# Kernel optimization log

Measured on AMD Instinct MI355X. Metric: run time of the kernel, lower is better.

## Reference

```python
import jax, jax.numpy as jnp
import numpy as np

INPUT_SIZE, HIDDEN, OUT = 2, 32, 1

def setup_inputs() -> dict:
    key = jax.random.key(0)
    ks = jax.random.split(key, 8)
    B, T = 2048, 512
    s_ih = 1.0 / np.sqrt(HIDDEN)
    return {
        "x": jax.random.normal(ks[0], (B, T, INPUT_SIZE), dtype=jnp.float32),
        "W_ih": jax.random.uniform(ks[1], (4 * HIDDEN, INPUT_SIZE), minval=-s_ih, maxval=s_ih, dtype=jnp.float32),
        "W_hh": jax.random.uniform(ks[2], (4 * HIDDEN, HIDDEN), minval=-s_ih, maxval=s_ih, dtype=jnp.float32),
        "b_ih": jax.random.uniform(ks[3], (4 * HIDDEN,), minval=-s_ih, maxval=s_ih, dtype=jnp.float32),
        "b_hh": jax.random.uniform(ks[4], (4 * HIDDEN,), minval=-s_ih, maxval=s_ih, dtype=jnp.float32),
        "W_fc": jax.random.uniform(ks[5], (OUT, HIDDEN), minval=-s_ih, maxval=s_ih, dtype=jnp.float32),
        "b_fc": jax.random.uniform(ks[6], (OUT,), minval=-s_ih, maxval=s_ih, dtype=jnp.float32),
    }

def _lstm(x, W_ih, W_hh, b_ih, b_hh):
    # x: [B, T, I]; PyTorch gate order: i, f, g, o
    B, T, _ = x.shape
    H = W_hh.shape[1]
    # precompute input projections for all timesteps: [T, B, 4H]
    xp = jnp.einsum('bti,gi->tbg', x, W_ih) + (b_ih + b_hh)

    def step(carry, xp_t):
        h, c = carry
        gates = xp_t + h @ W_hh.T  # [B, 4H]
        i, f, g, o = jnp.split(gates, 4, axis=-1)
        i = jax.nn.sigmoid(i)
        f = jax.nn.sigmoid(f)
        g = jnp.tanh(g)
        o = jax.nn.sigmoid(o)
        c = f * c + i * g
        h = o * jnp.tanh(c)
        return (h, c), h

    h0 = jnp.zeros((B, H), dtype=x.dtype)
    c0 = jnp.zeros((B, H), dtype=x.dtype)
    _, hs = jax.lax.scan(step, (h0, c0), xp)  # hs: [T, B, H]
    return jnp.transpose(hs, (1, 0, 2))  # [B, T, H]

def reference(x, W_ih, W_hh, b_ih, b_hh, W_fc, b_fc):
    lstm_out = _lstm(x, W_ih, W_hh, b_ih, b_hh)  # [B, T, H]
    return lstm_out @ W_fc.T + b_fc  # [B, T, OUT]
```

## Files before the change

kernel.cpp:

```cpp
#include <hip/hip_runtime.h>


#define BB 2048
#define TT 512
#define HH 32
#define CHUNK 64
#define HROW 33

typedef float v2f __attribute__((ext_vector_type(2)));
typedef float v4f __attribute__((ext_vector_type(4)));

__device__ __forceinline__ float sigm(float x) {
    return __builtin_amdgcn_rcpf(1.0f + __expf(-x));
}

__global__ __launch_bounds__(256, 2) void lstm_fused_kernel(
    const float* __restrict__ x,
    const float* __restrict__ W_ih,
    const float* __restrict__ W_hh,
    const float* __restrict__ b_ih,
    const float* __restrict__ b_hh,
    const float* __restrict__ W_fc,
    const float* __restrict__ b_fc,
    float* __restrict__ out)
{
    __shared__ float lds_x[4 * TT * 2];
    __shared__ float lds_h[4 * CHUNK * HROW];
    __shared__ __align__(16) float lds_bc[4][64];

    const int lane = threadIdx.x & 63;
    const int wv   = threadIdx.x >> 6;
    const int b    = blockIdx.x * 4 + wv;
    const bool low = (lane < 32);

    {
        const float4* xg = (const float4*)(x + (size_t)b * TT * 2);
        float4* xs = (float4*)(lds_x + wv * TT * 2);
        #pragma unroll
        for (int r = 0; r < 4; ++r) xs[r * 64 + lane] = xg[r * 64 + lane];
    }

    const int rlo = lane;
    const int rhi = lane + 64;
    const v2f wihl = ((const v2f*)W_ih)[rlo];
    const v2f wihh = ((const v2f*)W_ih)[rhi];
    const float bl = b_ih[rlo] + b_hh[rlo];
    const float bh = b_ih[rhi] + b_hh[rhi];

    v2f wloq[HH / 2], whiq[HH / 2];
    #pragma unroll
    for (int k = 0; k < HH / 2; ++k) {
        wloq[k] = ((const v2f*)(W_hh + rlo * HH))[k];
        whiq[k] = ((const v2f*)(W_hh + rhi * HH))[k];
    }

    float wfc[HH];
    #pragma unroll
    for (int u = 0; u < HH; ++u) wfc[u] = W_fc[u];
    const float bfc = b_fc[0];

    const float Mm = low ? 2.0f : 1.0f;
    const float Aa = low ? 2.0f : 1.0f;
    const float Bb = low ? -1.0f : 0.0f;

    float c = 0.0f;

    float* out_b = out + (size_t)b * TT;
    const v2f* xw = (const v2f*)(lds_x + wv * TT * 2);
    float* hb  = lds_h + wv * CHUNK * HROW;
    float* bcw = lds_bc[wv];
    const v4f* bcr = (const v4f*)bcw;

    bcw[lane] = 0.0f;
    __syncthreads();

    const v2f binitL = {bl, 0.0f};
    const v2f binitH = {bh, 0.0f};

    #pragma unroll 1
    for (int ch = 0; ch < TT / CHUNK; ++ch) {
        #pragma unroll 2
        for (int u = 0; u < CHUNK; ++u) {
            v4f hq[8];
            #pragma unroll
            for (int q = 0; q < 8; ++q) hq[q] = bcr[q];

            v2f xt = xw[ch * CHUNK + u];

            v2f aL0 = __builtin_elementwise_fma(xt, wihl, binitL);
            v2f aH0 = __builtin_elementwise_fma(xt, wihh, binitH);
            v2f aL1 = {0.0f, 0.0f};
            v2f aH1 = {0.0f, 0.0f};

            #pragma unroll
            for (int k = 0; k < HH / 2; ++k) {
                v2f hp = (k & 1)
                    ? __builtin_shufflevector(hq[k >> 1], hq[k >> 1], 2, 3)
                    : __builtin_shufflevector(hq[k >> 1], hq[k >> 1], 0, 1);
                if (k < HH / 4) {
                    aL0 = __builtin_elementwise_fma(hp, wloq[k], aL0);
                    aH0 = __builtin_elementwise_fma(hp, whiq[k], aH0);
                } else {
                    aL1 = __builtin_elementwise_fma(hp, wloq[k], aL1);
                    aH1 = __builtin_elementwise_fma(hp, whiq[k], aH1);
                }
            }
            v2f aL = aL0 + aL1;
            v2f aH = aH0 + aH1;
            float glo = aL.x + aL.y;
            float ghi = aH.x + aH.y;

            float alo = sigm(glo);
            float ahi = fmaf(Aa, sigm(Mm * ghi), Bb);

            float fsw = __shfl_xor(alo, 32);
            float osw = __shfl_xor(ahi, 32);

            float iv = low ? alo : fsw;
            float fv = low ? fsw : alo;
            float gv = low ? ahi : osw;
            float ov = low ? osw : ahi;

            c = fmaf(fv, c, iv * gv);
            float tc = fmaf(2.0f, sigm(2.0f * c), -1.0f);
            float hnew = ov * tc;

            float* wr = low ? (bcw + lane) : (hb + u * HROW + (lane - 32));
            *wr = hnew;
        }

        float acc = bfc;
        const float* row = hb + lane * HROW;
        #pragma unroll
        for (int u = 0; u < HH; ++u)
            acc = fmaf(row[u], wfc[u], acc);
        out_b[ch * CHUNK + lane] = acc;
    }
}

extern "C" void kernel_launch(void* const* d_in, const int* in_sizes, int n_in,
                              void* d_out, int out_size, void* d_ws, size_t ws_size,
                              hipStream_t stream) {
    const float* x    = (const float*)d_in[0];
    const float* W_ih = (const float*)d_in[1];
    const float* W_hh = (const float*)d_in[2];
    const float* b_ih = (const float*)d_in[3];
    const float* b_hh = (const float*)d_in[4];
    const float* W_fc = (const float*)d_in[5];
    const float* b_fc = (const float*)d_in[6];
    float* out = (float*)d_out;

    dim3 grid(BB / 4);
    dim3 block(256);
    lstm_fused_kernel<<<grid, block, 0, stream>>>(x, W_ih, W_hh, b_ih, b_hh,
                                                  W_fc, b_fc, out);
}
```

Baseline: 233.1 us.

## Broadcast hidden state via readlane into SGPRs instead of LDS round-trip

Each step previously wrote h to LDS and read it back as eight float4 broadcasts for the recurrent matvec. The new path instead reads each lane's new h with readlane into SGPR pairs and feeds them as scalar operands to inline-asm v_pk_fma_f32, taking LDS latency off the serial per-step dependency chain. In exchange it issues 32 readlanes per step, which run serially on the scalar path and add VALU-to-SGPR hazard waits, and it uses more SGPRs. Inline asm may also limit how the compiler schedules these instructions.

```diff
diff --git a/kernel.cpp b/kernel.cpp
--- a/kernel.cpp
+++ b/kernel.cpp
@@ -8,10 +8,14 @@
 #define HROW 33
 
 typedef float v2f __attribute__((ext_vector_type(2)));
-typedef float v4f __attribute__((ext_vector_type(4)));
 
 __device__ __forceinline__ float sigm(float x) {
     return __builtin_amdgcn_rcpf(1.0f + __expf(-x));
+}
+
+__device__ __forceinline__ v2f pkfma_s(v2f acc, unsigned long long h2, v2f w) {
+    asm("v_pk_fma_f32 %0, %1, %2, %0" : "+v"(acc) : "s"(h2), "v"(w));
+    return acc;
 }
 
 __global__ __launch_bounds__(256, 2) void lstm_fused_kernel(
@@ -25,8 +29,7 @@
     float* __restrict__ out)
 {
     __shared__ float lds_x[4 * TT * 2];
-    __shared__ float lds_h[4 * CHUNK * HROW];
-    __shared__ __align__(16) float lds_bc[4][64];
+    __shared__ float lds_h[4 * (CHUNK + 1) * HROW];
 
     const int lane = threadIdx.x & 63;
     const int wv   = threadIdx.x >> 6;
@@ -40,8 +43,7 @@
         for (int r = 0; r < 4; ++r) xs[r * 64 + lane] = xg[r * 64 + lane];
     }
 
-    const int rlo = lane;
-    const int rhi = lane + 64;
+    const int rlo = lane, rhi = lane + 64;
     const v2f wihl = ((const v2f*)W_ih)[rlo];
     const v2f wihh = ((const v2f*)W_ih)[rhi];
     const float bl = b_ih[rlo] + b_hh[rlo];
@@ -64,14 +66,14 @@
     const float Bb = low ? -1.0f : 0.0f;
 
     float c = 0.0f;
+    unsigned long long hprev[HH / 2];
+    #pragma unroll
+    for (int k = 0; k < HH / 2; ++k) hprev[k] = 0ull;
 
     float* out_b = out + (size_t)b * TT;
     const v2f* xw = (const v2f*)(lds_x + wv * TT * 2);
-    float* hb  = lds_h + wv * CHUNK * HROW;
-    float* bcw = lds_bc[wv];
-    const v4f* bcr = (const v4f*)bcw;
+    float* hb = lds_h + wv * (CHUNK + 1) * HROW;
 
-    bcw[lane] = 0.0f;
     __syncthreads();
 
     const v2f binitL = {bl, 0.0f};
@@ -81,10 +83,6 @@
     for (int ch = 0; ch < TT / CHUNK; ++ch) {
         #pragma unroll 2
         for (int u = 0; u < CHUNK; ++u) {
-            v4f hq[8];
-            #pragma unroll
-            for (int q = 0; q < 8; ++q) hq[q] = bcr[q];
-
             v2f xt = xw[ch * CHUNK + u];
 
             v2f aL0 = __builtin_elementwise_fma(xt, wihl, binitL);
@@ -93,17 +91,11 @@
             v2f aH1 = {0.0f, 0.0f};
 
             #pragma unroll
-            for (int k = 0; k < HH / 2; ++k) {
-                v2f hp = (k & 1)
-                    ? __builtin_shufflevector(hq[k >> 1], hq[k >> 1], 2, 3)
-                    : __builtin_shufflevector(hq[k >> 1], hq[k >> 1], 0, 1);
-                if (k < HH / 4) {
-                    aL0 = __builtin_elementwise_fma(hp, wloq[k], aL0);
-                    aH0 = __builtin_elementwise_fma(hp, whiq[k], aH0);
-                } else {
-                    aL1 = __builtin_elementwise_fma(hp, wloq[k], aL1);
-                    aH1 = __builtin_elementwise_fma(hp, whiq[k], aH1);
-                }
+            for (int k = 0; k < HH / 4; ++k) {
+                aL0 = pkfma_s(aL0, hprev[k],          wloq[k]);
+                aL1 = pkfma_s(aL1, hprev[k + HH/4],   wloq[k + HH/4]);
+                aH0 = pkfma_s(aH0, hprev[k],          whiq[k]);
+                aH1 = pkfma_s(aH1, hprev[k + HH/4],   whiq[k + HH/4]);
             }
             v2f aL = aL0 + aL1;
             v2f aH = aH0 + aH1;
@@ -113,27 +105,37 @@
             float alo = sigm(glo);
             float ahi = fmaf(Aa, sigm(Mm * ghi), Bb);
 
-            float fsw = __shfl_xor(alo, 32);
-            float osw = __shfl_xor(ahi, 32);
+            float p0 = __shfl_xor(alo, 32);
+            float p1 = __shfl_xor(ahi, 32);
 
-            float iv = low ? alo : fsw;
-            float fv = low ? fsw : alo;
-            float gv = low ? ahi : osw;
-            float ov = low ? osw : ahi;
+            float iv = low ? alo : p0;
+            float fv = low ? p0  : alo;
+            float gv = low ? ahi : p1;
+            float ov = low ? p1  : ahi;
 
             c = fmaf(fv, c, iv * gv);
             float tc = fmaf(2.0f, sigm(2.0f * c), -1.0f);
             float hnew = ov * tc;
 
-            float* wr = low ? (bcw + lane) : (hb + u * HROW + (lane - 32));
+            float* wr = low ? (hb + CHUNK * HROW + lane)
+                            : (hb + u * HROW + (lane - 32));
             *wr = hnew;
+
+            #pragma unroll
+            for (int k = 0; k < HH / 2; ++k) {
+                unsigned lo32 = (unsigned)__builtin_amdgcn_readlane(
+                    __float_as_int(hnew), 2 * k);
+                unsigned hi32 = (unsigned)__builtin_amdgcn_readlane(
+                    __float_as_int(hnew), 2 * k + 1);
+                hprev[k] = ((unsigned long long)hi32 << 32) | lo32;
+            }
         }
 
         float acc = bfc;
         const float* row = hb + lane * HROW;
         #pragma unroll
-        for (int u = 0; u < HH; ++u)
-            acc = fmaf(row[u], wfc[u], acc);
+        for (int u2 = 0; u2 < HH; ++u2)
+            acc = fmaf(row[u2], wfc[u2], acc);
         out_b[ch * CHUNK + lane] = acc;
     }
 }
```

Measured after the change: 285.7 us. +22.6%, slower.
